# Kernel optimization log

Hardware: AMD Instinct MI355X
Metric: run time of the kernel (lower is better)

The kernel has to match this reference:

```python
import jax, jax.numpy as jnp
import numpy as np

D_MODEL = 1024
NUM_HEADS = 16
D_K = D_MODEL // NUM_HEADS
B, S = 2, 2048


def setup_inputs() -> dict:
    key = jax.random.key(0)
    ks = jax.random.split(key, 11)
    sc = 1.0 / np.sqrt(D_MODEL)
    return {
        "query": jax.random.normal(ks[0], (B, S, D_MODEL), jnp.float32),
        "key": jax.random.normal(ks[1], (B, S, D_MODEL), jnp.float32),
        "value": jax.random.normal(ks[2], (B, S, D_MODEL), jnp.float32),
        "Wq": jax.random.normal(ks[3], (D_MODEL, D_MODEL), jnp.float32) * sc,
        "bq": jnp.zeros((D_MODEL,), jnp.float32),
        "Wk": jax.random.normal(ks[4], (D_MODEL, D_MODEL), jnp.float32) * sc,
        "bk": jnp.zeros((D_MODEL,), jnp.float32),
        "Wv": jax.random.normal(ks[5], (D_MODEL, D_MODEL), jnp.float32) * sc,
        "bv": jnp.zeros((D_MODEL,), jnp.float32),
        "Wo": jax.random.normal(ks[6], (D_MODEL, D_MODEL), jnp.float32) * sc,
        "bo": jnp.zeros((D_MODEL,), jnp.float32),
    }


def reference(query, key, value, Wq, bq, Wk, bk, Wv, bv, Wo, bo):
    b, sq, _ = query.shape
    # projections -> [B, H, S, d_k]
    def split_heads(x):
        return x.reshape(b, -1, NUM_HEADS, D_K).transpose(0, 2, 1, 3)

    q = split_heads(query @ Wq + bq)
    k = split_heads(key @ Wk + bk)
    v = split_heads(value @ Wv + bv)

    scores = jnp.einsum("bhqd,bhkd->bhqk", q, k) / np.sqrt(D_K).astype(np.float32)
    probs = jax.nn.softmax(scores, axis=-1)  # dropout p=0 (eval) -> identity
    attn = jnp.einsum("bhqk,bhkd->bhqd", probs, v)
    attn = attn.transpose(0, 2, 1, 3).reshape(b, sq, D_MODEL)
    out = attn @ Wo + bo
    return out, probs
```

## Files before the change

kernel.cpp:

```cpp
#include <hip/hip_runtime.h>


typedef __bf16 bf16x8 __attribute__((ext_vector_type(8)));
typedef float f32x4 __attribute__((ext_vector_type(4)));

typedef const unsigned int __attribute__((address_space(1))) as1c_uint;
typedef unsigned int __attribute__((address_space(3))) as3_uint;

#define S_LEN 2048
#define DM 1024
#define NH 16
#define DK 64
#define BATCH 2
#define M_ROWS 4096
#define KE 0.18033688f

__device__ __forceinline__ unsigned short f2bfu(float f) {
  union { __bf16 b; unsigned short u; } cv;
  cv.b = (__bf16)f;
  return cv.u;
}

__device__ __forceinline__ void gload_lds16(const void* g, void* l) {
  __builtin_amdgcn_global_load_lds((as1c_uint*)g, (as3_uint*)l, 16, 0, 0);
}

__global__ __launch_bounds__(256) void cvt3_kernel(
    const float* __restrict__ q, const float* __restrict__ k,
    const float* __restrict__ v, unsigned short* __restrict__ oq,
    unsigned short* __restrict__ ok_, unsigned short* __restrict__ ov) {
  const float* in = blockIdx.z == 0 ? q : (blockIdx.z == 1 ? k : v);
  unsigned short* out = blockIdx.z == 0 ? oq : (blockIdx.z == 1 ? ok_ : ov);
  size_t i = (size_t)blockIdx.x * 256 + threadIdx.x;
  float4 f = ((const float4*)in)[i];
  ushort4 u;
  u.x = f2bfu(f.x); u.y = f2bfu(f.y); u.z = f2bfu(f.z); u.w = f2bfu(f.w);
  ((ushort4*)out)[i] = u;
}

__global__ __launch_bounds__(256) void wtrans_kernel(
    const float* __restrict__ w0, const float* __restrict__ w1,
    const float* __restrict__ w2, const float* __restrict__ w3,
    unsigned short* __restrict__ o0, unsigned short* __restrict__ o1,
    unsigned short* __restrict__ o2, unsigned short* __restrict__ o3) {
  const float* W = blockIdx.z == 0 ? w0 : (blockIdx.z == 1 ? w1 : (blockIdx.z == 2 ? w2 : w3));
  unsigned short* WT = blockIdx.z == 0 ? o0 : (blockIdx.z == 1 ? o1 : (blockIdx.z == 2 ? o2 : o3));
  __shared__ float tile[32][33];
  int tx = threadIdx.x & 31, ty = threadIdx.x >> 5;
  int bx = blockIdx.x * 32, by = blockIdx.y * 32;
#pragma unroll
  for (int i = 0; i < 32; i += 8)
    tile[ty + i][tx] = W[(size_t)(by + ty + i) * DM + bx + tx];
  __syncthreads();
#pragma unroll
  for (int i = 0; i < 32; i += 8)
    WT[(size_t)(bx + ty + i) * DM + by + tx] = f2bfu(tile[tx][ty + i]);
}

template <int EPI>
__device__ __forceinline__ void gemm_core(const unsigned short* __restrict__ A,
                                          const unsigned short* __restrict__ BT,
                                          const float* __restrict__ bias,
                                          void* __restrict__ C) {
  __shared__ __attribute__((aligned(16))) unsigned short As[128 * 32];
  __shared__ __attribute__((aligned(16))) unsigned short Bs[128 * 32];
  const int tid = threadIdx.x;
  const int w = tid >> 6, l = tid & 63;
  const int wr = w >> 1, wc = w & 1;
  const int fr = l & 15, fq = l >> 4;
  const int m0 = blockIdx.y * 128, n0 = blockIdx.x * 128;
  const int srow = l >> 2;
  const int sk8 = (l & 3) * 8;
  f32x4 acc[4][4] = {};

  for (int k0 = 0; k0 < DM; k0 += 32) {
#pragma unroll
    for (int c = 0; c < 2; c++) {
      int r = c * 64 + w * 16;
      gload_lds16(A + (size_t)(m0 + r + srow) * DM + k0 + sk8, As + (size_t)r * 32);
      gload_lds16(BT + (size_t)(n0 + r + srow) * DM + k0 + sk8, Bs + (size_t)r * 32);
    }
    __syncthreads();
    bf16x8 af[4], bfv[4];
#pragma unroll
    for (int m = 0; m < 4; m++)
      af[m] = *(const bf16x8*)(As + (size_t)(wr * 64 + m * 16 + fr) * 32 + fq * 8);
#pragma unroll
    for (int n = 0; n < 4; n++)
      bfv[n] = *(const bf16x8*)(Bs + (size_t)(wc * 64 + n * 16 + fr) * 32 + fq * 8);
#pragma unroll
    for (int m = 0; m < 4; m++)
#pragma unroll
      for (int n = 0; n < 4; n++)
        acc[m][n] = __builtin_amdgcn_mfma_f32_16x16x32_bf16(af[m], bfv[n], acc[m][n], 0, 0, 0);
    __syncthreads();
  }

#pragma unroll
  for (int m = 0; m < 4; m++) {
#pragma unroll
    for (int n = 0; n < 4; n++) {
      const int col = n0 + wc * 64 + n * 16 + fr;
      const float bv = bias[col];
#pragma unroll
      for (int j = 0; j < 4; j++) {
        const int row = m0 + wr * 64 + m * 16 + fq * 4 + j;
        const float v = acc[m][n][j] + bv;
        if (EPI == 0) {
          ((float*)C)[(size_t)row * DM + col] = v;
        } else {
          const int b = row >> 11, s = row & (S_LEN - 1);
          const int h = col >> 6, d = col & (DK - 1);
          ((unsigned short*)C)[(((size_t)b * NH + h) * S_LEN + s) * DK + d] = f2bfu(v);
        }
      }
    }
  }
}

__global__ __launch_bounds__(256) void gemm_qkv_kernel(
    const unsigned short* __restrict__ xq, const unsigned short* __restrict__ xk,
    const unsigned short* __restrict__ xv, const unsigned short* __restrict__ wq,
    const unsigned short* __restrict__ wk, const unsigned short* __restrict__ wv,
    const float* __restrict__ bq, const float* __restrict__ bk,
    const float* __restrict__ bv, unsigned short* __restrict__ oq,
    unsigned short* __restrict__ okk, unsigned short* __restrict__ ov) {
  const int z = blockIdx.z;
  const unsigned short* A = z == 0 ? xq : (z == 1 ? xk : xv);
  const unsigned short* BT = z == 0 ? wq : (z == 1 ? wk : wv);
  const float* bias = z == 0 ? bq : (z == 1 ? bk : bv);
  unsigned short* C = z == 0 ? oq : (z == 1 ? okk : ov);
  gemm_core<1>(A, BT, bias, C);
}

__global__ __launch_bounds__(256) void gemm_out_kernel(
    const unsigned short* __restrict__ A, const unsigned short* __restrict__ BT,
    const float* __restrict__ bias, float* __restrict__ C) {
  gemm_core<0>(A, BT, bias, C);
}

__global__ __launch_bounds__(256) void vtrans_kernel(
    const unsigned short* __restrict__ V, unsigned short* __restrict__ VT) {
  __shared__ __attribute__((aligned(16))) unsigned short t[64][72];
  const int bh = blockIdx.y, s0 = blockIdx.x * 64;
  const unsigned short* v = V + ((size_t)bh * S_LEN + s0) * DK;
  const int tid = threadIdx.x;
#pragma unroll
  for (int i = 0; i < 4; i++) {
    int idx = tid + 256 * i;
    int r = idx >> 4, c4 = (idx & 15) * 4;
    *(ushort4*)&t[r][c4] = *(const ushort4*)(v + (size_t)r * DK + c4);
  }
  __syncthreads();
  unsigned short* o = VT + (size_t)bh * DK * S_LEN + s0;
#pragma unroll
  for (int i = 0; i < 4; i++) {
    int idx = tid + 256 * i;
    int d = idx >> 4, s4 = (idx & 15) * 4;
    ushort4 u;
    u.x = t[s4 + 0][d]; u.y = t[s4 + 1][d];
    u.z = t[s4 + 2][d]; u.w = t[s4 + 3][d];
    *(ushort4*)(o + (size_t)d * S_LEN + s4) = u;
  }
}

__global__ __launch_bounds__(256) void attn_kernel(
    const unsigned short* __restrict__ Qp, const unsigned short* __restrict__ Kp,
    const unsigned short* __restrict__ VT, float* __restrict__ probs,
    unsigned short* __restrict__ attnc) {
  const int flat = blockIdx.y * 32 + blockIdx.x;
  const int xcd = flat & 7, r = flat >> 3;
  const int bh = xcd * 4 + (r >> 5);
  const int tile = r & 31;
  const int w = threadIdx.x >> 6, l = threadIdx.x & 63;
  const int fr = l & 15, fq = l >> 4;
  const int q0 = tile * 64 + w * 16;
  const int qrow = q0 + fr;
  const unsigned short* Qh = Qp + (size_t)bh * S_LEN * DK;
  const unsigned short* Kh = Kp + (size_t)bh * S_LEN * DK;
  const unsigned short* Vh = VT + (size_t)bh * DK * S_LEN;
  float* ph = probs + (size_t)bh * S_LEN * S_LEN;

  __shared__ __attribute__((aligned(16))) unsigned short Sb[4][64 * 64];
  __shared__ __attribute__((aligned(16))) unsigned short Pl[4][16][40];

  const int srow8 = l >> 3;
  const int sgran = ((l & 7) ^ (l >> 3)) << 3;
  const int kr7 = fr & 7;

  bf16x8 qf[2];
  qf[0] = *(const bf16x8*)(Qh + (size_t)qrow * DK + fq * 8);
  qf[1] = *(const bf16x8*)(Qh + (size_t)qrow * DK + 32 + fq * 8);

  const int NIT = S_LEN / 64;

#define STAGE_P1(itn, buf)                                                    \
  {                                                                           \
    _Pragma("unroll") for (int i = 0; i < 2; i++)                             \
        gload_lds16(Kh + (size_t)((itn) * 64 + w * 16 + i * 8 + srow8) * DK + \
                        sgran,                                                \
                    &Sb[buf][(w * 16 + i * 8) * 64]);                         \
  }

  float ps4[4] = {0.f, 0.f, 0.f, 0.f};
  STAGE_P1(0, 0);
  STAGE_P1(1, 1);
  asm volatile("s_waitcnt vmcnt(2)" : : : "memory");
  __builtin_amdgcn_s_barrier();
  for (int it = 0; it < NIT; ++it) {
    const unsigned short* kcur = &Sb[it % 3][0];
    if (it + 2 < NIT) STAGE_P1(it + 2, (it + 2) % 3);
#pragma unroll
    for (int t = 0; t < 4; t++) {
      const int rk = t * 16 + fr;
      const bf16x8 a0 = *(const bf16x8*)&kcur[rk * 64 + ((fq ^ kr7) << 3)];
      const bf16x8 a1 = *(const bf16x8*)&kcur[rk * 64 + (((fq + 4) ^ kr7) << 3)];
      f32x4 s4 = {0.f, 0.f, 0.f, 0.f};
      s4 = __builtin_amdgcn_mfma_f32_16x16x32_bf16(a0, qf[0], s4, 0, 0, 0);
      s4 = __builtin_amdgcn_mfma_f32_16x16x32_bf16(a1, qf[1], s4, 0, 0, 0);
#pragma unroll
      for (int j = 0; j < 4; j++) ps4[j] += __builtin_amdgcn_exp2f(s4[j] * KE);
    }
    if (it + 1 < NIT) {
      if (it + 2 < NIT) {
        asm volatile("s_waitcnt vmcnt(2)" : : : "memory");
      } else {
        asm volatile("s_waitcnt vmcnt(0)" : : : "memory");
      }
      __builtin_amdgcn_s_barrier();
    }
  }
#undef STAGE_P1
  float psum = (ps4[0] + ps4[1]) + (ps4[2] + ps4[3]);
  psum += __shfl_xor(psum, 16, 64);
  psum += __shfl_xor(psum, 32, 64);
  const float pinv = 1.f / psum;
  __builtin_amdgcn_s_barrier();

  f32x4 oacc[4] = {};
  float* phrow = ph + (size_t)qrow * S_LEN + fq * 4;
#pragma unroll
  for (int i = 0; i < 2; i++) {
    gload_lds16(Kh + (size_t)(w * 16 + i * 8 + srow8) * DK + sgran,
                &Sb[0][(w * 16 + i * 8) * 64]);
    gload_lds16(Vh + (size_t)(w * 16 + i * 8 + srow8) * S_LEN + sgran,
                &Sb[2][(w * 16 + i * 8) * 64]);
  }
  asm volatile("s_waitcnt vmcnt(0)" : : : "memory");
  __builtin_amdgcn_s_barrier();
  for (int it = 0; it < S_LEN / 64; ++it) {
    const int cur = it & 1;
    const int skb = it * 64;
    if (it + 1 < S_LEN / 64) {
#pragma unroll
      for (int i = 0; i < 2; i++) {
        gload_lds16(Kh + (size_t)(skb + 64 + w * 16 + i * 8 + srow8) * DK + sgran,
                    &Sb[cur ^ 1][(w * 16 + i * 8) * 64]);
        gload_lds16(Vh + (size_t)(w * 16 + i * 8 + srow8) * S_LEN + (skb + 64) + sgran,
                    &Sb[2 + (cur ^ 1)][(w * 16 + i * 8) * 64]);
      }
    }
#pragma unroll
    for (int sub = 0; sub < 2; sub++) {
#pragma unroll
      for (int t = 0; t < 2; t++) {
        const int rk = sub * 32 + t * 16 + fr;
        const bf16x8 a0 = *(const bf16x8*)&Sb[cur][rk * 64 + ((fq ^ kr7) << 3)];
        const bf16x8 a1 = *(const bf16x8*)&Sb[cur][rk * 64 + (((fq + 4) ^ kr7) << 3)];
        f32x4 s4 = {0.f, 0.f, 0.f, 0.f};
        s4 = __builtin_amdgcn_mfma_f32_16x16x32_bf16(a0, qf[0], s4, 0, 0, 0);
        s4 = __builtin_amdgcn_mfma_f32_16x16x32_bf16(a1, qf[1], s4, 0, 0, 0);
        f32x4 pv;
        ushort4 pb;
#pragma unroll
        for (int j = 0; j < 4; j++) {
          const float p = __builtin_amdgcn_exp2f(s4[j] * KE) * pinv;
          pv[j] = p;
          ((unsigned short*)&pb)[j] = f2bfu(p);
        }
        __builtin_nontemporal_store(pv, (f32x4*)(phrow + skb + sub * 32 + t * 16));
        *(ushort4*)&Pl[w][fr][t * 16 + fq * 4] = pb;
      }
      const bf16x8 pa = *(const bf16x8*)&Pl[w][fr][fq * 8];
      __builtin_amdgcn_s_setprio(1);
#pragma unroll
      for (int n = 0; n < 4; n++) {
        const bf16x8 vf =
            *(const bf16x8*)&Sb[2 + cur][(n * 16 + fr) * 64 + (((sub * 4 + fq) ^ kr7) << 3)];
        oacc[n] = __builtin_amdgcn_mfma_f32_16x16x32_bf16(pa, vf, oacc[n], 0, 0, 0);
      }
      __builtin_amdgcn_s_setprio(0);
    }
    if (it + 1 < S_LEN / 64) {
      asm volatile("s_waitcnt vmcnt(8)" : : : "memory");
      __builtin_amdgcn_s_barrier();
    }
  }

  const int b = bh >> 4, h = bh & (NH - 1);
#pragma unroll
  for (int n = 0; n < 4; n++) {
#pragma unroll
    for (int j = 0; j < 4; j++) {
      const int row = q0 + fq * 4 + j, col = h * DK + n * 16 + fr;
      attnc[(size_t)((size_t)b * S_LEN + row) * DM + col] = f2bfu(oacc[n][j]);
    }
  }
}

extern "C" void kernel_launch(void* const* d_in, const int* in_sizes, int n_in,
                              void* d_out, int out_size, void* d_ws, size_t ws_size,
                              hipStream_t stream) {
  const float* query = (const float*)d_in[0];
  const float* key   = (const float*)d_in[1];
  const float* value = (const float*)d_in[2];
  const float* Wq = (const float*)d_in[3];
  const float* bq = (const float*)d_in[4];
  const float* Wk = (const float*)d_in[5];
  const float* bk = (const float*)d_in[6];
  const float* Wv = (const float*)d_in[7];
  const float* bv = (const float*)d_in[8];
  const float* Wo = (const float*)d_in[9];
  const float* bo = (const float*)d_in[10];

  char* ws = (char*)d_ws;
  const size_t XSZ = (size_t)M_ROWS * DM * 2;
  const size_t WSZ = (size_t)DM * DM * 2;
  unsigned short* xq  = (unsigned short*)(ws);
  unsigned short* xk  = (unsigned short*)(ws + XSZ);
  unsigned short* xv  = (unsigned short*)(ws + 2 * XSZ);
  unsigned short* wtq = (unsigned short*)(ws + 3 * XSZ);
  unsigned short* wtk = (unsigned short*)(ws + 3 * XSZ + WSZ);
  unsigned short* wtv = (unsigned short*)(ws + 3 * XSZ + 2 * WSZ);
  unsigned short* wto = (unsigned short*)(ws + 3 * XSZ + 3 * WSZ);
  unsigned short* qp  = (unsigned short*)(ws + 3 * XSZ + 4 * WSZ);
  unsigned short* kp  = (unsigned short*)(ws + 4 * XSZ + 4 * WSZ);
  unsigned short* vp  = (unsigned short*)(ws + 5 * XSZ + 4 * WSZ);
  unsigned short* vT    = xk;
  unsigned short* attnc = xq;

  float* out = (float*)d_out;
  float* probs = (float*)d_out + (size_t)BATCH * S_LEN * DM;

  cvt3_kernel<<<dim3(4096, 1, 3), 256, 0, stream>>>(query, key, value, xq, xk, xv);
  wtrans_kernel<<<dim3(32, 32, 4), 256, 0, stream>>>(Wq, Wk, Wv, Wo, wtq, wtk, wtv, wto);
  gemm_qkv_kernel<<<dim3(8, 32, 3), 256, 0, stream>>>(xq, xk, xv, wtq, wtk, wtv,
                                                      bq, bk, bv, qp, kp, vp);
  vtrans_kernel<<<dim3(32, 32), 256, 0, stream>>>(vp, vT);
  attn_kernel<<<dim3(32, 32), 256, 0, stream>>>(qp, kp, vT, probs, attnc);
  gemm_out_kernel<<<dim3(8, 32), 256, 0, stream>>>(attnc, wto, bo, out);
}
```

Baseline: 283.1 us.

## Process 32 query rows per wave and stage probs through LDS for coalesced stores

Each wave now handles two 16-row query fragments, so every K/V tile loaded into LDS is reused by twice as many queries. The grid is halved to 512 blocks of 128 query rows. Probabilities go into a float LDS buffer and are written to global memory as row-contiguous 16-byte chunks. The bf16 MFMA operand is built by converting from that buffer. This adds register pressure and LDS traffic, and leaves fewer blocks to fill the CUs.

```diff
diff --git a/kernel.cpp b/kernel.cpp
--- a/kernel.cpp
+++ b/kernel.cpp
@@ -168,29 +168,31 @@
     const unsigned short* __restrict__ Qp, const unsigned short* __restrict__ Kp,
     const unsigned short* __restrict__ VT, float* __restrict__ probs,
     unsigned short* __restrict__ attnc) {
-  const int flat = blockIdx.y * 32 + blockIdx.x;
+  const int flat = blockIdx.x;
   const int xcd = flat & 7, r = flat >> 3;
-  const int bh = xcd * 4 + (r >> 5);
-  const int tile = r & 31;
+  const int bh = xcd * 4 + (r >> 4);
+  const int tile = r & 15;
   const int w = threadIdx.x >> 6, l = threadIdx.x & 63;
   const int fr = l & 15, fq = l >> 4;
-  const int q0 = tile * 64 + w * 16;
-  const int qrow = q0 + fr;
+  const int q0 = tile * 128 + w * 32;
   const unsigned short* Qh = Qp + (size_t)bh * S_LEN * DK;
   const unsigned short* Kh = Kp + (size_t)bh * S_LEN * DK;
   const unsigned short* Vh = VT + (size_t)bh * DK * S_LEN;
   float* ph = probs + (size_t)bh * S_LEN * S_LEN;
 
   __shared__ __attribute__((aligned(16))) unsigned short Sb[4][64 * 64];
-  __shared__ __attribute__((aligned(16))) unsigned short Pl[4][16][40];
+  __shared__ __attribute__((aligned(16))) float Pf[4][2][16][33];
 
   const int srow8 = l >> 3;
   const int sgran = ((l & 7) ^ (l >> 3)) << 3;
   const int kr7 = fr & 7;
 
-  bf16x8 qf[2];
-  qf[0] = *(const bf16x8*)(Qh + (size_t)qrow * DK + fq * 8);
-  qf[1] = *(const bf16x8*)(Qh + (size_t)qrow * DK + 32 + fq * 8);
+  bf16x8 qf[2][2];
+#pragma unroll
+  for (int f = 0; f < 2; f++) {
+    qf[f][0] = *(const bf16x8*)(Qh + (size_t)(q0 + f * 16 + fr) * DK + fq * 8);
+    qf[f][1] = *(const bf16x8*)(Qh + (size_t)(q0 + f * 16 + fr) * DK + 32 + fq * 8);
+  }
 
   const int NIT = S_LEN / 64;
 
@@ -202,7 +204,7 @@
                     &Sb[buf][(w * 16 + i * 8) * 64]);                         \
   }
 
-  float ps4[4] = {0.f, 0.f, 0.f, 0.f};
+  float ps[2][4] = {};
   STAGE_P1(0, 0);
   STAGE_P1(1, 1);
   asm volatile("s_waitcnt vmcnt(2)" : : : "memory");
@@ -215,11 +217,14 @@
       const int rk = t * 16 + fr;
       const bf16x8 a0 = *(const bf16x8*)&kcur[rk * 64 + ((fq ^ kr7) << 3)];
       const bf16x8 a1 = *(const bf16x8*)&kcur[rk * 64 + (((fq + 4) ^ kr7) << 3)];
-      f32x4 s4 = {0.f, 0.f, 0.f, 0.f};
-      s4 = __builtin_amdgcn_mfma_f32_16x16x32_bf16(a0, qf[0], s4, 0, 0, 0);
-      s4 = __builtin_amdgcn_mfma_f32_16x16x32_bf16(a1, qf[1], s4, 0, 0, 0);
-#pragma unroll
-      for (int j = 0; j < 4; j++) ps4[j] += __builtin_amdgcn_exp2f(s4[j] * KE);
+#pragma unroll
+      for (int f = 0; f < 2; f++) {
+        f32x4 s4 = {0.f, 0.f, 0.f, 0.f};
+        s4 = __builtin_amdgcn_mfma_f32_16x16x32_bf16(a0, qf[f][0], s4, 0, 0, 0);
+        s4 = __builtin_amdgcn_mfma_f32_16x16x32_bf16(a1, qf[f][1], s4, 0, 0, 0);
+#pragma unroll
+        for (int j = 0; j < 4; j++) ps[f][j] += __builtin_amdgcn_exp2f(s4[j] * KE);
+      }
     }
     if (it + 1 < NIT) {
       if (it + 2 < NIT) {
@@ -231,14 +236,19 @@
     }
   }
 #undef STAGE_P1
-  float psum = (ps4[0] + ps4[1]) + (ps4[2] + ps4[3]);
-  psum += __shfl_xor(psum, 16, 64);
-  psum += __shfl_xor(psum, 32, 64);
-  const float pinv = 1.f / psum;
+  float pinv[2];
+#pragma unroll
+  for (int f = 0; f < 2; f++) {
+    float psum = (ps[f][0] + ps[f][1]) + (ps[f][2] + ps[f][3]);
+    psum += __shfl_xor(psum, 16, 64);
+    psum += __shfl_xor(psum, 32, 64);
+    pinv[f] = 1.f / psum;
+  }
   __builtin_amdgcn_s_barrier();
 
-  f32x4 oacc[4] = {};
-  float* phrow = ph + (size_t)qrow * S_LEN + fq * 4;
+  f32x4 oacc[2][4] = {};
+  const int strow = l >> 3;
+  const int stcol = (l & 7) * 4;
 #pragma unroll
   for (int i = 0; i < 2; i++) {
     gload_lds16(Kh + (size_t)(w * 16 + i * 8 + srow8) * DK + sgran,
@@ -267,29 +277,50 @@
         const int rk = sub * 32 + t * 16 + fr;
         const bf16x8 a0 = *(const bf16x8*)&Sb[cur][rk * 64 + ((fq ^ kr7) << 3)];
         const bf16x8 a1 = *(const bf16x8*)&Sb[cur][rk * 64 + (((fq + 4) ^ kr7) << 3)];
-        f32x4 s4 = {0.f, 0.f, 0.f, 0.f};
-        s4 = __builtin_amdgcn_mfma_f32_16x16x32_bf16(a0, qf[0], s4, 0, 0, 0);
-        s4 = __builtin_amdgcn_mfma_f32_16x16x32_bf16(a1, qf[1], s4, 0, 0, 0);
-        f32x4 pv;
-        ushort4 pb;
+#pragma unroll
+        for (int f = 0; f < 2; f++) {
+          f32x4 s4 = {0.f, 0.f, 0.f, 0.f};
+          s4 = __builtin_amdgcn_mfma_f32_16x16x32_bf16(a0, qf[f][0], s4, 0, 0, 0);
+          s4 = __builtin_amdgcn_mfma_f32_16x16x32_bf16(a1, qf[f][1], s4, 0, 0, 0);
+          f32x4 pv;
+#pragma unroll
+          for (int j = 0; j < 4; j++)
+            pv[j] = __builtin_amdgcn_exp2f(s4[j] * KE) * pinv[f];
+          *(f32x4*)&Pf[w][f][fr][t * 16 + fq * 4] = pv;
+        }
+      }
+      bf16x8 pa[2];
+#pragma unroll
+      for (int f = 0; f < 2; f++) {
+        const f32x4 plo = *(const f32x4*)&Pf[w][f][fr][fq * 8];
+        const f32x4 phi = *(const f32x4*)&Pf[w][f][fr][fq * 8 + 4];
 #pragma unroll
         for (int j = 0; j < 4; j++) {
-          const float p = __builtin_amdgcn_exp2f(s4[j] * KE) * pinv;
-          pv[j] = p;
-          ((unsigned short*)&pb)[j] = f2bfu(p);
+          pa[f][j] = (__bf16)plo[j];
+          pa[f][j + 4] = (__bf16)phi[j];
         }
-        __builtin_nontemporal_store(pv, (f32x4*)(phrow + skb + sub * 32 + t * 16));
-        *(ushort4*)&Pl[w][fr][t * 16 + fq * 4] = pb;
-      }
-      const bf16x8 pa = *(const bf16x8*)&Pl[w][fr][fq * 8];
+      }
       __builtin_amdgcn_s_setprio(1);
 #pragma unroll
       for (int n = 0; n < 4; n++) {
         const bf16x8 vf =
             *(const bf16x8*)&Sb[2 + cur][(n * 16 + fr) * 64 + (((sub * 4 + fq) ^ kr7) << 3)];
-        oacc[n] = __builtin_amdgcn_mfma_f32_16x16x32_bf16(pa, vf, oacc[n], 0, 0, 0);
+#pragma unroll
+        for (int f = 0; f < 2; f++)
+          oacc[f][n] = __builtin_amdgcn_mfma_f32_16x16x32_bf16(pa[f], vf, oacc[f][n], 0, 0, 0);
       }
       __builtin_amdgcn_s_setprio(0);
+#pragma unroll
+      for (int f = 0; f < 2; f++) {
+#pragma unroll
+        for (int i = 0; i < 2; i++) {
+          const int row16 = i * 8 + strow;
+          const f32x4 pv4 = *(const f32x4*)&Pf[w][f][row16][stcol];
+          __builtin_nontemporal_store(
+              pv4, (f32x4*)(ph + (size_t)(q0 + f * 16 + row16) * S_LEN + skb +
+                            sub * 32 + stcol));
+        }
+      }
     }
     if (it + 1 < S_LEN / 64) {
       asm volatile("s_waitcnt vmcnt(8)" : : : "memory");
@@ -299,11 +330,14 @@
 
   const int b = bh >> 4, h = bh & (NH - 1);
 #pragma unroll
-  for (int n = 0; n < 4; n++) {
-#pragma unroll
-    for (int j = 0; j < 4; j++) {
-      const int row = q0 + fq * 4 + j, col = h * DK + n * 16 + fr;
-      attnc[(size_t)((size_t)b * S_LEN + row) * DM + col] = f2bfu(oacc[n][j]);
+  for (int f = 0; f < 2; f++) {
+#pragma unroll
+    for (int n = 0; n < 4; n++) {
+#pragma unroll
+      for (int j = 0; j < 4; j++) {
+        const int row = q0 + f * 16 + fq * 4 + j, col = h * DK + n * 16 + fr;
+        attnc[(size_t)((size_t)b * S_LEN + row) * DM + col] = f2bfu(oacc[f][n][j]);
+      }
     }
   }
 }
@@ -347,6 +381,6 @@
   gemm_qkv_kernel<<<dim3(8, 32, 3), 256, 0, stream>>>(xq, xk, xv, wtq, wtk, wtv,
                                                       bq, bk, bv, qp, kp, vp);
   vtrans_kernel<<<dim3(32, 32), 256, 0, stream>>>(vp, vT);
-  attn_kernel<<<dim3(32, 32), 256, 0, stream>>>(qp, kp, vT, probs, attnc);
+  attn_kernel<<<dim3(512), 256, 0, stream>>>(qp, kp, vT, probs, attnc);
   gemm_out_kernel<<<dim3(8, 32), 256, 0, stream>>>(attnc, wto, bo, out);
 }
```

After: 259.3 us. 8.4% less time.
